# Optimization experiments

Hardware: AMD Instinct MI355X
Metric: run time of the kernel (lower is better)

The kernel has to match this reference:

```python
import jax, jax.numpy as jnp
import numpy as np


def setup_inputs() -> dict:
    key = jax.random.key(0)
    k1, k2, k3 = jax.random.split(key, 3)
    B, S, D_IN, D_OUT = 8, 512, 4096, 16384
    x = jax.random.normal(k1, (B, S, D_IN), dtype=jnp.float32)
    # int8 weights stored as int32 values in [-128, 127] (int8 semantics)
    weight_int8 = jax.random.randint(k2, (D_OUT, D_IN), -128, 128, dtype=jnp.int32)
    # per-tensor scale, e.g. max_abs/127 of an fp32 weight with std ~0.02
    weight_scale = jnp.float32(0.02 * 4.0 / 127.0)
    bias = jax.random.normal(k3, (D_OUT,), dtype=jnp.float32) * 0.01
    return {"x": x, "weight_int8": weight_int8, "weight_scale": weight_scale, "bias": bias}


def reference(x, weight_int8, weight_scale, bias):
    # dequantize: materialize fp32 weight (per-tensor scale, zero_point = 0)
    weight_fp32 = weight_int8.astype(jnp.float32) * weight_scale  # [O, I]
    # F.linear: y = x @ W^T + b
    out = jnp.einsum("bsi,oi->bso", x, weight_fp32) + bias
    return out
```

## Files before the change

kernel.cpp:

```cpp
#include <hip/hip_runtime.h>
#include <stdint.h>
#include <stddef.h>

typedef __attribute__((ext_vector_type(4))) int       i32x4;
typedef __attribute__((ext_vector_type(8))) short     bf16x8;
typedef __attribute__((ext_vector_type(4))) float     f32x4;
typedef __attribute__((ext_vector_type(4))) float     f32x4v;
typedef __attribute__((ext_vector_type(4))) unsigned short u16x4;

__device__ __forceinline__ unsigned short f2bf(float f) {
    union { float f; unsigned u; } v; v.f = f;
    unsigned r = v.u + 0x7FFFu + ((v.u >> 16) & 1u);
    return (unsigned short)(r >> 16);
}

__device__ __forceinline__ void gload_lds16(const void* g, void* l) {
    __builtin_amdgcn_global_load_lds(
        (const __attribute__((address_space(1))) void*)(g),
        (__attribute__((address_space(3))) void*)(l), 16, 0, 0);
}

__device__ __forceinline__ int pack4(float a, float b, float c, float d, float inv) {
    int r0 = ((int)rintf(a * inv)) & 255;
    int r1 = ((int)rintf(b * inv)) & 255;
    int r2 = ((int)rintf(c * inv)) & 255;
    int r3 = ((int)rintf(d * inv)) & 255;
    return r0 | (r1 << 8) | (r2 << 16) | (r3 << 24);
}

__global__ void cvt_x_q8(const float* __restrict__ x, signed char* __restrict__ xq,
                         float* __restrict__ sx, int K) {
    const int row = blockIdx.x;
    const int t   = threadIdx.x;
    const float* xr = x + (size_t)row * K;
    const int ng = K / 1024;

    f32x4v v[8];
    float am = 0.f;
#pragma unroll
    for (int i = 0; i < 8; ++i) {
        if (i < ng) {
            v[i] = __builtin_nontemporal_load(&((const f32x4v*)xr)[i * 256 + t]);
            am = fmaxf(am, fmaxf(fmaxf(fabsf(v[i][0]), fabsf(v[i][1])),
                                 fmaxf(fabsf(v[i][2]), fabsf(v[i][3]))));
        }
    }
#pragma unroll
    for (int m = 32; m >= 1; m >>= 1) am = fmaxf(am, __shfl_xor(am, m, 64));
    __shared__ float red[4];
    const int w = t >> 6;
    if ((t & 63) == 0) red[w] = am;
    __syncthreads();
    am = fmaxf(fmaxf(red[0], red[1]), fmaxf(red[2], red[3]));

    const float inv = (am > 0.f) ? 127.0f / am : 0.f;
    if (t == 0) sx[row] = (am > 0.f) ? am / 127.0f : 0.f;

    int* oq = (int*)(xq + (size_t)row * K);
#pragma unroll
    for (int i = 0; i < 8; ++i)
        if (i < ng) oq[i * 256 + t] = pack4(v[i][0], v[i][1], v[i][2], v[i][3], inv);
}

__global__ void cvt_w_q8(const int* __restrict__ w, signed char* __restrict__ o, int n4) {
    int i = blockIdx.x * blockDim.x + threadIdx.x;
    int stride = gridDim.x * blockDim.x;
    for (; i < n4; i += stride) {
        i32x4 a = __builtin_nontemporal_load(&((const i32x4*)w)[i]);
        ((int*)o)[i] = (a[0] & 255) | ((a[1] & 255) << 8) | ((a[2] & 255) << 16) | ((a[3] & 255) << 24);
    }
}

#define BM8 256
#define BN8 256
#define BKQ 128

__global__ __launch_bounds__(512, 2) void gemm8p_i8(
    const signed char* __restrict__ A,
    const signed char* __restrict__ Bw,
    const float* __restrict__ sx,
    const float* __restrict__ scale_p,
    const float* __restrict__ bias,
    float* __restrict__ C,
    int M, int N, int K)
{
    __shared__ __align__(16) char smem[131072];

    const int t    = threadIdx.x;
    const int lane = t & 63;
    const int w    = t >> 6;
    const int wm   = w >> 2;
    const int wn   = w & 3;

    int nwg = gridDim.x, bid = blockIdx.x;
    int swz = ((nwg & 7) == 0) ? ((bid & 7) * (nwg >> 3) + (bid >> 3)) : bid;
    const int ntn  = N / BN8;
    const int row0 = (swz / ntn) * BM8;
    const int col0 = (swz % ntn) * BN8;

    const int Kb = K;
    const int NT = K / BKQ;

    const int srow = w * 8 + (lane >> 3);
    const int sc2  = ((lane & 7) ^ (lane >> 3)) * 16;
    const int ldsLaneOff = w * 1024 + lane * 16;

    const char* aG = (const char*)A + (size_t)(row0 + srow) * Kb + sc2;
    const char* bG = (const char*)Bw + (size_t)(col0 + srow) * Kb + sc2;

    const int q    = lane >> 4;
    const int lr   = lane & 15;
    const int swzr = (lr & 7) << 4;

    i32x4 acc[8][4] = {};
    i32x4 aF[4][2], aS[4][2], bF[2][2], bS[2][2];

#define STG(gbase, h, tj, buf, region) do {                                   \
    const char* _g = (gbase) + (size_t)(h) * 128 * Kb + (size_t)(tj) * 128;   \
    char* _l = &smem[(buf) * 65536 + (region) * 16384 + ldsLaneOff];          \
    gload_lds16(_g, _l);                                                      \
    gload_lds16(_g + (size_t)64 * Kb, _l + 8192);                             \
} while (0)

#define RDA(buf, mi, ks) \
    (*(const i32x4*)&smem[(buf) * 65536 + wm * 16384 + ((mi) * 16 + lr) * 128 \
                          + ((((ks) << 6) | (q << 4)) ^ swzr)])
#define RDB(buf, nj, ks) \
    (*(const i32x4*)&smem[(buf) * 65536 + (2 + (wn >> 1)) * 16384              \
                          + ((wn & 1) * 64 + (nj) * 16 + lr) * 128             \
                          + ((((ks) << 6) | (q << 4)) ^ swzr)])

#define MFMA_(a, b, c) (c) = __builtin_amdgcn_mfma_i32_16x16x64_i8((a), (b), (c), 0, 0, 0)
#define BAR() __builtin_amdgcn_s_barrier()
#define FENCE() asm volatile("" ::: "memory")
#define VM4() asm volatile("s_waitcnt vmcnt(4)" ::: "memory")
#define VM0() asm volatile("s_waitcnt vmcnt(0)" ::: "memory")
#define VMNONE() do { } while (0)

#define TILE_STEP(tt, bb, stB, stA2, VMW) do {                                        \
                              \
    _Pragma("unroll") for (int mi = 0; mi < 4; ++mi) {                                \
        aF[mi][0] = RDA(bb, mi, 0); aF[mi][1] = RDA(bb, mi, 1); }                     \
    _Pragma("unroll") for (int nj = 0; nj < 2; ++nj) {                                \
        bF[nj][0] = RDB(bb, nj, 0); bF[nj][1] = RDB(bb, nj, 1); }                     \
    if (stB) STG(bG, 0, (tt) + 1, (bb) ^ 1, 2);                                       \
    __builtin_amdgcn_s_setprio(1);                                                    \
    _Pragma("unroll") for (int mi = 0; mi < 4; ++mi)                                  \
    _Pragma("unroll") for (int nj = 0; nj < 2; ++nj) {                                \
        MFMA_(aF[mi][0], bF[nj][0], acc[mi][nj]);                                     \
        MFMA_(aF[mi][1], bF[nj][1], acc[mi][nj]); }                                   \
    __builtin_amdgcn_s_setprio(0);                                                    \
                                 \
    _Pragma("unroll") for (int nj = 0; nj < 2; ++nj) {                                \
        bS[nj][0] = RDB(bb, 2 + nj, 0); bS[nj][1] = RDB(bb, 2 + nj, 1); }             \
    if (stB) STG(bG, 1, (tt) + 1, (bb) ^ 1, 3);                                       \
    __builtin_amdgcn_s_setprio(1);                                                    \
    _Pragma("unroll") for (int mi = 0; mi < 4; ++mi)                                  \
    _Pragma("unroll") for (int nj = 0; nj < 2; ++nj) {                                \
        MFMA_(aF[mi][0], bS[nj][0], acc[mi][2 + nj]);                                 \
        MFMA_(aF[mi][1], bS[nj][1], acc[mi][2 + nj]); }                               \
    __builtin_amdgcn_s_setprio(0);                                                    \
                                                \
    _Pragma("unroll") for (int mi = 0; mi < 4; ++mi) {                                \
        aS[mi][0] = RDA(bb, 4 + mi, 0); aS[mi][1] = RDA(bb, 4 + mi, 1); }             \
    __builtin_amdgcn_s_setprio(1);                                                    \
    _Pragma("unroll") for (int mi = 0; mi < 4; ++mi)                                  \
    _Pragma("unroll") for (int nj = 0; nj < 2; ++nj) {                                \
        MFMA_(aS[mi][0], bS[nj][0], acc[4 + mi][2 + nj]);                             \
        MFMA_(aS[mi][1], bS[nj][1], acc[4 + mi][2 + nj]); }                           \
    __builtin_amdgcn_s_setprio(0);                                                    \
    BAR(); FENCE();              \
              \
    _Pragma("unroll") for (int nj = 0; nj < 2; ++nj) {                                \
        bF[nj][0] = RDB(bb, nj, 0); bF[nj][1] = RDB(bb, nj, 1); }                     \
    if (stA2) { STG(aG, 0, (tt) + 2, (bb), 0); STG(aG, 1, (tt) + 2, (bb), 1); }       \
    __builtin_amdgcn_s_setprio(1);                                                    \
    _Pragma("unroll") for (int mi = 0; mi < 4; ++mi)                                  \
    _Pragma("unroll") for (int nj = 0; nj < 2; ++nj) {                                \
        MFMA_(aS[mi][0], bF[nj][0], acc[4 + mi][nj]);                                 \
        MFMA_(aS[mi][1], bF[nj][1], acc[4 + mi][nj]); }                               \
    __builtin_amdgcn_s_setprio(0);                                                    \
    VMW();                                                                            \
    BAR(); FENCE();              \
} while (0)

    STG(aG, 0, 0, 0, 0); STG(aG, 1, 0, 0, 1);
    STG(bG, 0, 0, 0, 2); STG(bG, 1, 0, 0, 3);
    STG(aG, 0, 1, 1, 0); STG(aG, 1, 1, 1, 1);
    VM4();
    BAR(); FENCE();

    for (int tt = 0; tt < NT - 2; tt += 2) {
        TILE_STEP(tt,     0, 1, 1, VM4);
        TILE_STEP(tt + 1, 1, 1, 1, VM4);
    }
    TILE_STEP(NT - 2, 0, 1, 0, VM0);
    TILE_STEP(NT - 1, 1, 0, 0, VMNONE);

    const float s = scale_p[0];
    float bv[4];
#pragma unroll
    for (int nj = 0; nj < 4; ++nj) bv[nj] = bias[col0 + wn * 64 + nj * 16 + lr];
#pragma unroll
    for (int mi = 0; mi < 8; ++mi) {
        const int rbase = row0 + wm * 128 + mi * 16 + q * 4;
        float sxr[4];
#pragma unroll
        for (int j = 0; j < 4; ++j) sxr[j] = sx[rbase + j] * s;
#pragma unroll
        for (int nj = 0; nj < 4; ++nj) {
            const int col = col0 + wn * 64 + nj * 16 + lr;
#pragma unroll
            for (int j = 0; j < 4; ++j)
                __builtin_nontemporal_store((float)acc[mi][nj][j] * sxr[j] + bv[nj],
                                            &C[(size_t)(rbase + j) * N + col]);
        }
    }
#undef STG
#undef RDA
#undef RDB
#undef TILE_STEP
}

#define BM 128
#define BN 128
#define BK 64

__global__ __launch_bounds__(256, 2) void gemm_fused(
    const float* __restrict__ A,
    const int* __restrict__ Bw,
    const float* __restrict__ scale_p,
    const float* __restrict__ bias,
    float* __restrict__ C,
    int M, int N, int K)
{
    __shared__ unsigned short As[BM * BK];
    __shared__ unsigned short Bs[BN * BK];
    const int t = threadIdx.x, lane = t & 63, w = t >> 6;
    const int wm = w >> 1, wn = w & 1;
    int nwg = gridDim.x, bid = blockIdx.x;
    int swz = (nwg % 8 == 0) ? ((bid & 7) * (nwg >> 3) + (bid >> 3)) : bid;
    const int ntn = N / BN;
    const int row0 = (swz / ntn) * BM, col0 = (swz % ntn) * BN;
    f32x4 acc[4][4] = {};
    const int lr = lane & 15, lkbase = (lane >> 4) * 8;

    for (int kt = 0; kt < K; kt += BK) {
#pragma unroll
        for (int i = 0; i < 8; ++i) {
            const int r = i * 16 + (t >> 4), c = (t & 15) * 4;
            f32x4v v = *(const f32x4v*)&A[(size_t)(row0 + r) * K + kt + c];
            u16x4 o; o[0] = f2bf(v[0]); o[1] = f2bf(v[1]); o[2] = f2bf(v[2]); o[3] = f2bf(v[3]);
            *(u16x4*)&As[r * BK + c] = o;
        }
#pragma unroll
        for (int i = 0; i < 8; ++i) {
            const int r = i * 16 + (t >> 4), c = (t & 15) * 4;
            i32x4 v = *(const i32x4*)&Bw[(size_t)(col0 + r) * K + kt + c];
            u16x4 o; o[0] = f2bf((float)v[0]); o[1] = f2bf((float)v[1]);
                     o[2] = f2bf((float)v[2]); o[3] = f2bf((float)v[3]);
            *(u16x4*)&Bs[r * BK + c] = o;
        }
        __syncthreads();
#pragma unroll
        for (int ks = 0; ks < 2; ++ks) {
            const int lk = lkbase + ks * 8 * 4;
            bf16x8 af[4], bfr[4];
#pragma unroll
            for (int m = 0; m < 4; ++m) af[m] = *(const bf16x8*)&As[(wm * 64 + m * 16 + lr) * BK + lkbase + ks * 32];
#pragma unroll
            for (int n = 0; n < 4; ++n) bfr[n] = *(const bf16x8*)&Bs[(wn * 64 + n * 16 + lr) * BK + lkbase + ks * 32];
#pragma unroll
            for (int m = 0; m < 4; ++m)
#pragma unroll
                for (int n = 0; n < 4; ++n)
                    acc[m][n] = __builtin_amdgcn_mfma_f32_16x16x32_bf16(af[m], bfr[n], acc[m][n], 0, 0, 0);
            (void)lk;
        }
        __syncthreads();
    }
    const float s = scale_p[0];
    const int lq4 = (lane >> 4) * 4;
#pragma unroll
    for (int m = 0; m < 4; ++m)
#pragma unroll
        for (int n = 0; n < 4; ++n) {
            const int col = col0 + wn * 64 + n * 16 + lr;
            const float bv = bias[col];
#pragma unroll
            for (int j = 0; j < 4; ++j) {
                const int row = row0 + wm * 64 + m * 16 + lq4 + j;
                C[(size_t)row * N + col] = acc[m][n][j] * s + bv;
            }
        }
}

extern "C" void kernel_launch(void* const* d_in, const int* in_sizes, int n_in,
                              void* d_out, int out_size, void* d_ws, size_t ws_size,
                              hipStream_t stream) {
    const float* x     = (const float*)d_in[0];
    const int*   w8    = (const int*)d_in[1];
    const float* scale = (const float*)d_in[2];
    const float* bias  = (const float*)d_in[3];
    float* out = (float*)d_out;

    const int N = in_sizes[3];
    const int K = (int)((long)in_sizes[1] / N);
    const int M = (int)((long)in_sizes[0] / K);

    const size_t needA = (size_t)M * K;
    const size_t needB = (size_t)N * K;
    const size_t needS = (size_t)M * sizeof(float);
    const int NT = K / BKQ;

    const bool okShape = (M % BM8 == 0) && (N % BN8 == 0) && (K % BKQ == 0) &&
                         (K % 1024 == 0) && (K / 1024 <= 8) &&
                         (NT >= 4) && ((NT & 1) == 0);

    if (okShape && ws_size >= needA + needB + needS) {
        signed char* Aq = (signed char*)d_ws;
        signed char* Bq = Aq + needA;
        float*       sx = (float*)(Bq + needB);
        cvt_x_q8<<<M, 256, 0, stream>>>(x, Aq, sx, K);
        cvt_w_q8<<<4096, 256, 0, stream>>>(w8, Bq, (int)((size_t)N * K / 4));
        const int nblocks = (M / BM8) * (N / BN8);
        gemm8p_i8<<<nblocks, 512, 0, stream>>>(Aq, Bq, sx, scale, bias, out, M, N, K);
    } else {
        const int nblocks = (M / BM) * (N / BN);
        gemm_fused<<<nblocks, 256, 0, stream>>>(x, w8, scale, bias, out, M, N, K);
    }
}
```

Measured before the change: 341.1 us.

## Switch int8 GEMM to 32x32x32 MFMA and remap tile swizzle

Replaces the 16x16x64 int8 MFMA with the 32x32x32 variant. LDS fragment reads, the accumulator layout (i32x16) and the epilogue row mapping are reworked to match. This cuts LDS read traffic per MFMA, since each larger tile reuses its operands more. The workgroup-to-tile mapping is changed to group M tiles into 8 XCD-aligned stripes when divisible, for better L2 reuse of weights. The epilogue also drops nontemporal stores in favor of plain stores, and the 32x32 MFMA has different latency and register pressure.

```diff
diff --git a/kernel.cpp b/kernel.cpp
--- a/kernel.cpp
+++ b/kernel.cpp
@@ -2,11 +2,12 @@
 #include <stdint.h>
 #include <stddef.h>
 
-typedef __attribute__((ext_vector_type(4))) int       i32x4;
-typedef __attribute__((ext_vector_type(8))) short     bf16x8;
-typedef __attribute__((ext_vector_type(4))) float     f32x4;
-typedef __attribute__((ext_vector_type(4))) float     f32x4v;
-typedef __attribute__((ext_vector_type(4))) unsigned short u16x4;
+typedef __attribute__((ext_vector_type(4)))  int   i32x4;
+typedef __attribute__((ext_vector_type(16))) int   i32x16;
+typedef __attribute__((ext_vector_type(8)))  short bf16x8;
+typedef __attribute__((ext_vector_type(4)))  float f32x4;
+typedef __attribute__((ext_vector_type(4)))  float f32x4v;
+typedef __attribute__((ext_vector_type(4)))  unsigned short u16x4;
 
 __device__ __forceinline__ unsigned short f2bf(float f) {
     union { float f; unsigned u; } v; v.f = f;
@@ -92,11 +93,23 @@
     const int wm   = w >> 2;
     const int wn   = w & 3;
 
+    const int ntn = N / BN8;
+    const int ntm = M / BM8;
     int nwg = gridDim.x, bid = blockIdx.x;
-    int swz = ((nwg & 7) == 0) ? ((bid & 7) * (nwg >> 3) + (bid >> 3)) : bid;
-    const int ntn  = N / BN8;
-    const int row0 = (swz / ntn) * BM8;
-    const int col0 = (swz % ntn) * BN8;
+    int tm, tn;
+    if (((nwg & 7) == 0) && (ntm % 8 == 0)) {
+        const int x = bid & 7, c = bid >> 3;
+        const int tmB = ntm >> 3;
+        tm = x * tmB + (c % tmB);
+        tn = c / tmB;
+    } else if ((nwg & 7) == 0) {
+        int swz = (bid & 7) * (nwg >> 3) + (bid >> 3);
+        tm = swz / ntn; tn = swz % ntn;
+    } else {
+        tm = bid / ntn; tn = bid % ntn;
+    }
+    const int row0 = tm * BM8;
+    const int col0 = tn * BN8;
 
     const int Kb = K;
     const int NT = K / BKQ;
@@ -108,12 +121,12 @@
     const char* aG = (const char*)A + (size_t)(row0 + srow) * Kb + sc2;
     const char* bG = (const char*)Bw + (size_t)(col0 + srow) * Kb + sc2;
 
-    const int q    = lane >> 4;
-    const int lr   = lane & 15;
-    const int swzr = (lr & 7) << 4;
-
-    i32x4 acc[8][4] = {};
-    i32x4 aF[4][2], aS[4][2], bF[2][2], bS[2][2];
+    const int l31  = lane & 31;
+    const int hi   = lane >> 5;
+    const int swzr = (l31 & 7) << 4;
+
+    i32x16 acc[4][2] = {};
+    i32x4 aF[2][4], aS[2][4], bF[4], bS[4];
 
 #define STG(gbase, h, tj, buf, region) do {                                   \
     const char* _g = (gbase) + (size_t)(h) * 128 * Kb + (size_t)(tj) * 128;   \
@@ -122,15 +135,15 @@
     gload_lds16(_g + (size_t)64 * Kb, _l + 8192);                             \
 } while (0)
 
-#define RDA(buf, mi, ks) \
-    (*(const i32x4*)&smem[(buf) * 65536 + wm * 16384 + ((mi) * 16 + lr) * 128 \
-                          + ((((ks) << 6) | (q << 4)) ^ swzr)])
+#define RDA(buf, mt, ks) \
+    (*(const i32x4*)&smem[(buf) * 65536 + wm * 16384 + ((mt) * 32 + l31) * 128 \
+                          + ((((ks) << 5) | (hi << 4)) ^ swzr)])
 #define RDB(buf, nj, ks) \
     (*(const i32x4*)&smem[(buf) * 65536 + (2 + (wn >> 1)) * 16384              \
-                          + ((wn & 1) * 64 + (nj) * 16 + lr) * 128             \
-                          + ((((ks) << 6) | (q << 4)) ^ swzr)])
-
-#define MFMA_(a, b, c) (c) = __builtin_amdgcn_mfma_i32_16x16x64_i8((a), (b), (c), 0, 0, 0)
+                          + ((wn & 1) * 64 + (nj) * 32 + l31) * 128            \
+                          + ((((ks) << 5) | (hi << 4)) ^ swzr)])
+
+#define MFMA_(a, b, c) (c) = __builtin_amdgcn_mfma_i32_32x32x32_i8((a), (b), (c), 0, 0, 0)
 #define BAR() __builtin_amdgcn_s_barrier()
 #define FENCE() asm volatile("" ::: "memory")
 #define VM4() asm volatile("s_waitcnt vmcnt(4)" ::: "memory")
@@ -138,50 +151,43 @@
 #define VMNONE() do { } while (0)
 
 #define TILE_STEP(tt, bb, stB, stA2, VMW) do {                                        \
-                              \
-    _Pragma("unroll") for (int mi = 0; mi < 4; ++mi) {                                \
-        aF[mi][0] = RDA(bb, mi, 0); aF[mi][1] = RDA(bb, mi, 1); }                     \
-    _Pragma("unroll") for (int nj = 0; nj < 2; ++nj) {                                \
-        bF[nj][0] = RDB(bb, nj, 0); bF[nj][1] = RDB(bb, nj, 1); }                     \
+                        \
+    _Pragma("unroll") for (int mi = 0; mi < 2; ++mi)                                  \
+    _Pragma("unroll") for (int ks = 0; ks < 4; ++ks) aF[mi][ks] = RDA(bb, mi, ks);    \
+    _Pragma("unroll") for (int ks = 0; ks < 4; ++ks) bF[ks] = RDB(bb, 0, ks);         \
     if (stB) STG(bG, 0, (tt) + 1, (bb) ^ 1, 2);                                       \
     __builtin_amdgcn_s_setprio(1);                                                    \
-    _Pragma("unroll") for (int mi = 0; mi < 4; ++mi)                                  \
-    _Pragma("unroll") for (int nj = 0; nj < 2; ++nj) {                                \
-        MFMA_(aF[mi][0], bF[nj][0], acc[mi][nj]);                                     \
-        MFMA_(aF[mi][1], bF[nj][1], acc[mi][nj]); }                                   \
+    _Pragma("unroll") for (int ks = 0; ks < 4; ++ks)                                  \
+    _Pragma("unroll") for (int mi = 0; mi < 2; ++mi)                                  \
+        MFMA_(aF[mi][ks], bF[ks], acc[mi][0]);                                        \
     __builtin_amdgcn_s_setprio(0);                                                    \
-                                 \
-    _Pragma("unroll") for (int nj = 0; nj < 2; ++nj) {                                \
-        bS[nj][0] = RDB(bb, 2 + nj, 0); bS[nj][1] = RDB(bb, 2 + nj, 1); }             \
+                                  \
+    _Pragma("unroll") for (int ks = 0; ks < 4; ++ks) bS[ks] = RDB(bb, 1, ks);         \
     if (stB) STG(bG, 1, (tt) + 1, (bb) ^ 1, 3);                                       \
     __builtin_amdgcn_s_setprio(1);                                                    \
-    _Pragma("unroll") for (int mi = 0; mi < 4; ++mi)                                  \
-    _Pragma("unroll") for (int nj = 0; nj < 2; ++nj) {                                \
-        MFMA_(aF[mi][0], bS[nj][0], acc[mi][2 + nj]);                                 \
-        MFMA_(aF[mi][1], bS[nj][1], acc[mi][2 + nj]); }                               \
+    _Pragma("unroll") for (int ks = 0; ks < 4; ++ks)                                  \
+    _Pragma("unroll") for (int mi = 0; mi < 2; ++mi)                                  \
+        MFMA_(aF[mi][ks], bS[ks], acc[mi][1]);                                        \
     __builtin_amdgcn_s_setprio(0);                                                    \
-                                                \
-    _Pragma("unroll") for (int mi = 0; mi < 4; ++mi) {                                \
-        aS[mi][0] = RDA(bb, 4 + mi, 0); aS[mi][1] = RDA(bb, 4 + mi, 1); }             \
+                                               \
+    _Pragma("unroll") for (int mi = 0; mi < 2; ++mi)                                  \
+    _Pragma("unroll") for (int ks = 0; ks < 4; ++ks) aS[mi][ks] = RDA(bb, 2 + mi, ks);\
     __builtin_amdgcn_s_setprio(1);                                                    \
-    _Pragma("unroll") for (int mi = 0; mi < 4; ++mi)                                  \
-    _Pragma("unroll") for (int nj = 0; nj < 2; ++nj) {                                \
-        MFMA_(aS[mi][0], bS[nj][0], acc[4 + mi][2 + nj]);                             \
-        MFMA_(aS[mi][1], bS[nj][1], acc[4 + mi][2 + nj]); }                           \
+    _Pragma("unroll") for (int ks = 0; ks < 4; ++ks)                                  \
+    _Pragma("unroll") for (int mi = 0; mi < 2; ++mi)                                  \
+        MFMA_(aS[mi][ks], bS[ks], acc[2 + mi][1]);                                    \
     __builtin_amdgcn_s_setprio(0);                                                    \
-    BAR(); FENCE();              \
-              \
-    _Pragma("unroll") for (int nj = 0; nj < 2; ++nj) {                                \
-        bF[nj][0] = RDB(bb, nj, 0); bF[nj][1] = RDB(bb, nj, 1); }                     \
+    BAR(); FENCE();                                                                   \
+                \
+    _Pragma("unroll") for (int ks = 0; ks < 4; ++ks) bF[ks] = RDB(bb, 0, ks);         \
     if (stA2) { STG(aG, 0, (tt) + 2, (bb), 0); STG(aG, 1, (tt) + 2, (bb), 1); }       \
     __builtin_amdgcn_s_setprio(1);                                                    \
-    _Pragma("unroll") for (int mi = 0; mi < 4; ++mi)                                  \
-    _Pragma("unroll") for (int nj = 0; nj < 2; ++nj) {                                \
-        MFMA_(aS[mi][0], bF[nj][0], acc[4 + mi][nj]);                                 \
-        MFMA_(aS[mi][1], bF[nj][1], acc[4 + mi][nj]); }                               \
+    _Pragma("unroll") for (int ks = 0; ks < 4; ++ks)                                  \
+    _Pragma("unroll") for (int mi = 0; mi < 2; ++mi)                                  \
+        MFMA_(aS[mi][ks], bF[ks], acc[2 + mi][0]);                                    \
     __builtin_amdgcn_s_setprio(0);                                                    \
     VMW();                                                                            \
-    BAR(); FENCE();              \
+    BAR(); FENCE();                                                                   \
 } while (0)
 
     STG(aG, 0, 0, 0, 0); STG(aG, 1, 0, 0, 1);
@@ -198,22 +204,24 @@
     TILE_STEP(NT - 1, 1, 0, 0, VMNONE);
 
     const float s = scale_p[0];
-    float bv[4];
-#pragma unroll
-    for (int nj = 0; nj < 4; ++nj) bv[nj] = bias[col0 + wn * 64 + nj * 16 + lr];
-#pragma unroll
-    for (int mi = 0; mi < 8; ++mi) {
-        const int rbase = row0 + wm * 128 + mi * 16 + q * 4;
-        float sxr[4];
-#pragma unroll
-        for (int j = 0; j < 4; ++j) sxr[j] = sx[rbase + j] * s;
-#pragma unroll
-        for (int nj = 0; nj < 4; ++nj) {
-            const int col = col0 + wn * 64 + nj * 16 + lr;
-#pragma unroll
-            for (int j = 0; j < 4; ++j)
-                __builtin_nontemporal_store((float)acc[mi][nj][j] * sxr[j] + bv[nj],
-                                            &C[(size_t)(rbase + j) * N + col]);
+    float bvv[2];
+#pragma unroll
+    for (int nj = 0; nj < 2; ++nj) bvv[nj] = bias[col0 + wn * 64 + nj * 32 + l31];
+#pragma unroll
+    for (int mi = 0; mi < 4; ++mi) {
+        const int rb = row0 + wm * 128 + mi * 32;
+        float sxv[16];
+#pragma unroll
+        for (int j = 0; j < 16; ++j)
+            sxv[j] = sx[rb + (j & 3) + 8 * (j >> 2) + 4 * hi] * s;
+#pragma unroll
+        for (int nj = 0; nj < 2; ++nj) {
+            const int col = col0 + wn * 64 + nj * 32 + l31;
+#pragma unroll
+            for (int j = 0; j < 16; ++j) {
+                const int row = rb + (j & 3) + 8 * (j >> 2) + 4 * hi;
+                C[(size_t)row * N + col] = (float)acc[mi][nj][j] * sxv[j] + bvv[nj];
+            }
         }
     }
 #undef STG
@@ -264,7 +272,6 @@
         __syncthreads();
 #pragma unroll
         for (int ks = 0; ks < 2; ++ks) {
-            const int lk = lkbase + ks * 8 * 4;
             bf16x8 af[4], bfr[4];
 #pragma unroll
             for (int m = 0; m < 4; ++m) af[m] = *(const bf16x8*)&As[(wm * 64 + m * 16 + lr) * BK + lkbase + ks * 32];
@@ -275,7 +282,6 @@
 #pragma unroll
                 for (int n = 0; n < 4; ++n)
                     acc[m][n] = __builtin_amdgcn_mfma_f32_16x16x32_bf16(af[m], bfr[n], acc[m][n], 0, 0, 0);
-            (void)lk;
         }
         __syncthreads();
     }
```

New measurement: 356.8 us. +4.6%, slower.
